# Kernel tuning notes

Hardware: AMD Instinct MI355X
Metric: run time of the kernel (lower is better)

Reference implementation:

```python
import jax, jax.numpy as jnp
import numpy as np

D = 4096
N = 8192


def fwht(x):
    """Fast Walsh-Hadamard Transform (orthonormal, divided by sqrt(d)).

    log2(d) butterfly stages, each a single vectorized add/sub over the
    full tensor. Loop bound is static (log2 of trailing dim), jit-safe.
    """
    d = x.shape[-1]
    leading = x.shape[:-1]
    h = 1
    while h < d:
        x = x.reshape(*leading, d // (2 * h), 2, h)
        a = x[..., 0, :]
        b = x[..., 1, :]
        x = jnp.stack([a + b, a - b], axis=-2).reshape(*leading, d)
        h *= 2
    return x * jnp.asarray(d, x.dtype) ** -0.5


def setup_inputs() -> dict:
    key = jax.random.key(0)
    kx, ks = jax.random.split(key)
    x = jax.random.normal(kx, (N, D), dtype=jnp.float32)
    # deterministic random +/-1 sign vector (buffer of RHTRotation)
    signs = (jax.random.randint(ks, (D,), 0, 2).astype(jnp.float32) * 2.0 - 1.0)
    return {"x": x, "signs": signs}


def reference(x, signs):
    # randomized_hadamard: y = H @ (D x) / sqrt(d), D = diag(signs)
    return fwht(x * signs)
```

## Files before the change

### kernel.cpp

```cpp
#include <hip/hip_runtime.h>

#define D 4096

__device__ __forceinline__ void fwht16(float v[16]) {
#pragma unroll
    for (int s = 1; s < 16; s <<= 1) {
#pragma unroll
        for (int i = 0; i < 16; i++) {
            if (!(i & s)) {
                float a = v[i], b = v[i ^ s];
                v[i]     = a + b;
                v[i ^ s] = a - b;
            }
        }
    }
}

__global__ __launch_bounds__(256) void fwht_kernel(const float* __restrict__ x,
                                                   const float* __restrict__ signs,
                                                   float* __restrict__ out) {
    __shared__ float lds[4352];

    const int t = threadIdx.x;
    const long row = blockIdx.x;
    const float* __restrict__ xr = x + row * (long)D;
    float* __restrict__ orow = out + row * (long)D;

    float v[16];

    {
        const float4* __restrict__ xv = (const float4*)(xr + t * 16);
        const float4* __restrict__ sv = (const float4*)(signs + t * 16);
#pragma unroll
        for (int k = 0; k < 4; k++) {
            float4 a = xv[k];
            float4 s = sv[k];
            v[4 * k + 0] = a.x * s.x;
            v[4 * k + 1] = a.y * s.y;
            v[4 * k + 2] = a.z * s.z;
            v[4 * k + 3] = a.w * s.w;
        }
    }
    fwht16(v);

#pragma unroll
    for (int b = 0; b < 16; b++) lds[17 * t + b] = v[b];
    __syncthreads();

    {
        const int a2 = t >> 4, b = t & 15;
        const int base = a2 * 272 + b;
#pragma unroll
        for (int a1 = 0; a1 < 16; a1++) v[a1] = lds[base + a1 * 17];
        fwht16(v);
#pragma unroll
        for (int a1 = 0; a1 < 16; a1++) lds[base + a1 * 17] = v[a1];
    }
    __syncthreads();

    {
        const int base = (t >> 4) * 17 + (t & 15);
#pragma unroll
        for (int a2 = 0; a2 < 16; a2++) v[a2] = lds[base + a2 * 272];
        fwht16(v);
        const float scale = 1.0f / 64.0f;
#pragma unroll
        for (int a2 = 0; a2 < 16; a2++) orow[a2 * 256 + t] = v[a2] * scale;
    }
}

extern "C" void kernel_launch(void* const* d_in, const int* in_sizes, int n_in,
                              void* d_out, int out_size, void* d_ws, size_t ws_size,
                              hipStream_t stream) {
    const float* x = (const float*)d_in[0];
    const float* signs = (const float*)d_in[1];
    float* out = (float*)d_out;
    const int rows = in_sizes[0] / D;
    fwht_kernel<<<dim3(rows), dim3(256), 0, stream>>>(x, signs, out);
}
```

Measured before the change: 227.9 us.

## Process one row per wavefront using register butterflies and cross-lane shuffles

Reorganizes the transform so each 64-lane wavefront owns a whole row, holding 64 values per lane. Butterfly stages within a float4 and across register groups are done in registers, and the six middle stages use xor shuffles instead of LDS round trips and block barriers. Loads and stores become coalesced float4 accesses. The trade is higher register pressure and many cross-lane shuffle operations, which may be costly if lowered to ds_bpermute.

```diff
diff --git a/kernel.cpp b/kernel.cpp
--- a/kernel.cpp
+++ b/kernel.cpp
@@ -2,70 +2,78 @@
 
 #define D 4096
 
-__device__ __forceinline__ void fwht16(float v[16]) {
+__global__ __launch_bounds__(256, 4) void fwht_kernel(const float* __restrict__ x,
+                                                      const float* __restrict__ signs,
+                                                      float* __restrict__ out,
+                                                      int rows) {
+    const int lane = threadIdx.x & 63;
+    const int wid = threadIdx.x >> 6;
+    const long row = (long)blockIdx.x * 4 + wid;
+    if (row >= rows) return;
+
+    const float4* __restrict__ xv = (const float4*)(x + row * (long)D);
+    const float4* __restrict__ sv = (const float4*)signs;
+    float4* __restrict__ ov = (float4*)(out + row * (long)D);
+
+    float v[64];
+
+#pragma unroll
+    for (int k = 0; k < 16; k++) {
+        float4 a = xv[k * 64 + lane];
+        float4 s = sv[k * 64 + lane];
+        v[4 * k + 0] = a.x * s.x;
+        v[4 * k + 1] = a.y * s.y;
+        v[4 * k + 2] = a.z * s.z;
+        v[4 * k + 3] = a.w * s.w;
+    }
+
+#pragma unroll
+    for (int k = 0; k < 16; k++) {
+        float a0 = v[4 * k + 0], a1 = v[4 * k + 1];
+        float a2 = v[4 * k + 2], a3 = v[4 * k + 3];
+        float b0 = a0 + a1, b1 = a0 - a1;
+        float b2 = a2 + a3, b3 = a2 - a3;
+        v[4 * k + 0] = b0 + b2;
+        v[4 * k + 1] = b1 + b3;
+        v[4 * k + 2] = b0 - b2;
+        v[4 * k + 3] = b1 - b3;
+    }
+
+#pragma unroll
+    for (int s = 1; s < 64; s <<= 1) {
+        const float sgn = (lane & s) ? -1.0f : 1.0f;
+#pragma unroll
+        for (int i = 0; i < 64; i++) {
+            float p = __shfl_xor(v[i], s, 64);
+            v[i] = fmaf(sgn, v[i], p);
+        }
+    }
+
 #pragma unroll
     for (int s = 1; s < 16; s <<= 1) {
 #pragma unroll
-        for (int i = 0; i < 16; i++) {
-            if (!(i & s)) {
-                float a = v[i], b = v[i ^ s];
-                v[i]     = a + b;
-                v[i ^ s] = a - b;
+        for (int k = 0; k < 16; k++) {
+            if (!(k & s)) {
+#pragma unroll
+                for (int j = 0; j < 4; j++) {
+                    float a = v[4 * k + j];
+                    float b = v[4 * (k ^ s) + j];
+                    v[4 * k + j] = a + b;
+                    v[4 * (k ^ s) + j] = a - b;
+                }
             }
         }
     }
-}
 
-__global__ __launch_bounds__(256) void fwht_kernel(const float* __restrict__ x,
-                                                   const float* __restrict__ signs,
-                                                   float* __restrict__ out) {
-    __shared__ float lds[4352];
-
-    const int t = threadIdx.x;
-    const long row = blockIdx.x;
-    const float* __restrict__ xr = x + row * (long)D;
-    float* __restrict__ orow = out + row * (long)D;
-
-    float v[16];
-
-    {
-        const float4* __restrict__ xv = (const float4*)(xr + t * 16);
-        const float4* __restrict__ sv = (const float4*)(signs + t * 16);
+    const float scale = 1.0f / 64.0f;
 #pragma unroll
-        for (int k = 0; k < 4; k++) {
-            float4 a = xv[k];
-            float4 s = sv[k];
-            v[4 * k + 0] = a.x * s.x;
-            v[4 * k + 1] = a.y * s.y;
-            v[4 * k + 2] = a.z * s.z;
-            v[4 * k + 3] = a.w * s.w;
-        }
-    }
-    fwht16(v);
-
-#pragma unroll
-    for (int b = 0; b < 16; b++) lds[17 * t + b] = v[b];
-    __syncthreads();
-
-    {
-        const int a2 = t >> 4, b = t & 15;
-        const int base = a2 * 272 + b;
-#pragma unroll
-        for (int a1 = 0; a1 < 16; a1++) v[a1] = lds[base + a1 * 17];
-        fwht16(v);
-#pragma unroll
-        for (int a1 = 0; a1 < 16; a1++) lds[base + a1 * 17] = v[a1];
-    }
-    __syncthreads();
-
-    {
-        const int base = (t >> 4) * 17 + (t & 15);
-#pragma unroll
-        for (int a2 = 0; a2 < 16; a2++) v[a2] = lds[base + a2 * 272];
-        fwht16(v);
-        const float scale = 1.0f / 64.0f;
-#pragma unroll
-        for (int a2 = 0; a2 < 16; a2++) orow[a2 * 256 + t] = v[a2] * scale;
+    for (int k = 0; k < 16; k++) {
+        float4 r;
+        r.x = v[4 * k + 0] * scale;
+        r.y = v[4 * k + 1] * scale;
+        r.z = v[4 * k + 2] * scale;
+        r.w = v[4 * k + 3] * scale;
+        ov[k * 64 + lane] = r;
     }
 }
 
@@ -76,5 +84,6 @@
     const float* signs = (const float*)d_in[1];
     float* out = (float*)d_out;
     const int rows = in_sizes[0] / D;
-    fwht_kernel<<<dim3(rows), dim3(256), 0, stream>>>(x, signs, out);
+    const int blocks = (rows + 3) / 4;
+    fwht_kernel<<<dim3(blocks), dim3(256), 0, stream>>>(x, signs, out, rows);
 }
```

Result: slower. 244.6 us (+7.3%).
